# Optimization experiments

Measured on AMD Instinct MI355X. Metric: run time of the kernel, lower is better.

## Reference

```python
import jax, jax.numpy as jnp
import numpy as np

BETA = 0.2


def setup_inputs() -> dict:
    key = jax.random.key(0)
    k1, k2 = jax.random.split(key)
    B, C, H, W = 32, 64, 64, 64  # C == H == W required by the original reshape/permute
    K, D = 512, 64               # num_embeddings, embedding_dim (D == C)
    quant_input = jax.random.normal(k1, (B, C, H, W), dtype=jnp.float32)
    codebook = jax.random.normal(k2, (K, D), dtype=jnp.float32)
    return {"quant_input": quant_input, "codebook": codebook}


def reference(quant_input, codebook):
    B, C, H, W = quant_input.shape
    # (B,C,H,W) -> (B,HW,C)
    x = jnp.transpose(quant_input, (0, 2, 3, 1)).reshape(B, H * W, C)
    # squared euclidean distances (argmin identical to cdist argmin)
    x_sq = jnp.sum(x * x, axis=-1, keepdims=True)          # (B,HW,1)
    e_sq = jnp.sum(codebook * codebook, axis=-1)            # (K,)
    dist = x_sq - 2.0 * jnp.einsum('bnd,kd->bnk', x, codebook) + e_sq  # (B,HW,K)
    encoding_indices = jnp.argmin(dist, axis=-1)            # (B,HW)
    # gather codes, then the original (buggy-but-faithful) reshape/permute
    quant_out = codebook[encoding_indices.reshape(-1)]      # (B*HW, D)
    quant_out = quant_out.reshape(quant_input.shape)        # (B,C,H,W) layout
    quant_out = jnp.transpose(quant_out, (0, 3, 1, 2))      # (B,W,C,H)
    commitment_loss = jnp.mean((jax.lax.stop_gradient(quant_out) - quant_input) ** 2)
    codebook_loss = jnp.mean((quant_out - jax.lax.stop_gradient(quant_input)) ** 2)
    loss = codebook_loss + BETA * commitment_loss
    # straight-through estimator
    quant_out = quant_input + jax.lax.stop_gradient(quant_out - quant_input)
    encoding_indices = encoding_indices.reshape(-1, quant_out.shape[-2], quant_out.shape[-1])
    return quant_out, loss, encoding_indices
```

## Files before the change

### kernel.cpp

```cpp
#include <hip/hip_runtime.h>
#include <math.h>

#define K_CODES 512
#define DIM 64
#define NPTS (32 * 4096)
#define NQ (NPTS * DIM)
#define BPTS 128
#define TAU 2.0e-3f

typedef _Float16 f16x8 __attribute__((ext_vector_type(8)));
typedef float f32x4 __attribute__((ext_vector_type(4)));


__global__ void finalize_kernel(float* __restrict__ loss) {
    loss[0] = 1.2f * loss[0] / 8388608.0f;
}

__global__ __launch_bounds__(64) void prep_kernel(const float* __restrict__ cb,
                                                  _Float16* __restrict__ blob,
                                                  float* __restrict__ shalfg,
                                                  float* __restrict__ loss) {
    int k = blockIdx.x, d = threadIdx.x;
    if (k == 0 && d == 0) loss[0] = 0.0f;
    float e = cb[k * DIM + d];
    _Float16 hi = (_Float16)e;
    _Float16 lo = (_Float16)(e - (float)hi);
    int cf = k >> 4, col = k & 15;
    int q = d >> 5, dd = d & 31, kg = dd >> 3, j = dd & 7;
    size_t base = ((size_t)(cf * 4 + q) * 64 + (kg * 16 + col)) * 8 + j;
    blob[base] = hi;
    blob[base + 2 * 64 * 8] = lo;
    float s = e * e;
#pragma unroll
    for (int m = 32; m; m >>= 1) s += __shfl_xor(s, m);
    if (d == 0) shalfg[k] = 0.5f * s;
}

__global__ __launch_bounds__(256, 1) void vq_fused(const float* __restrict__ qin,
                                                   const float* __restrict__ cb,
                                                   const _Float16* __restrict__ blob,
                                                   const float* __restrict__ shalfg,
                                                   float* __restrict__ out,
                                                   float* __restrict__ loss_acc,
                                                   float* __restrict__ idx_out) {
    __shared__ float shs[K_CODES];
    __shared__ int sfinal[BPTS];
    __shared__ float wsum[4];

    const int tid = threadIdx.x, lane = tid & 63, w = tid >> 6;
    const int row16 = lane & 15, kg = lane >> 4;
    const int wp = w * 32;
    const int n0 = blockIdx.x * BPTS;
    const int b = n0 >> 12, hw0 = n0 & 4095;
    const float* qbase = qin + ((size_t)b << 18) + hw0;
    const f16x8* blp = (const f16x8*)blob + lane;

    shs[tid] = shalfg[tid];
    shs[tid + 256] = shalfg[tid + 256];

    f16x8 ah0[2], ah1[2], al0[2], al1[2];
#pragma unroll
    for (int rr = 0; rr < 2; ++rr) {
        const float* xb = qbase + (wp + rr * 16 + row16);
#pragma unroll
        for (int j = 0; j < 8; ++j) {
            float xa = xb[(size_t)(kg * 8 + j) << 12];
            float xc = xb[(size_t)(32 + kg * 8 + j) << 12];
            _Float16 ha = (_Float16)xa, hc = (_Float16)xc;
            ah0[rr][j] = ha; al0[rr][j] = (_Float16)(xa - (float)ha);
            ah1[rr][j] = hc; al1[rr][j] = (_Float16)(xc - (float)hc);
        }
    }
    __syncthreads();

    float b1[8], b2[8];
    int k1[8];
#pragma unroll
    for (int sl = 0; sl < 8; ++sl) { b1[sl] = -INFINITY; b2[sl] = -INFINITY; k1[sl] = 0; }

#define LOADB(P0, P1, P2, P3, CF)              \
    {                                          \
        P0 = blp[((CF) * 4 + 0) * 64];         \
        P1 = blp[((CF) * 4 + 1) * 64];         \
        P2 = blp[((CF) * 4 + 2) * 64];         \
        P3 = blp[((CF) * 4 + 3) * 64];         \
    }
#define CONSUME(CF, B0, B1, BL0, BL1)                                              \
    {                                                                              \
        float sh = shs[(CF) * 16 + row16];                                         \
        f32x4 acA0 = {-sh, -sh, -sh, -sh}, acB0 = {0.f, 0.f, 0.f, 0.f};            \
        f32x4 acA1 = acA0, acB1 = acB0;                                            \
        acA0 = __builtin_amdgcn_mfma_f32_16x16x32_f16(ah0[0], B0, acA0, 0, 0, 0);  \
        acB0 = __builtin_amdgcn_mfma_f32_16x16x32_f16(al0[0], B0, acB0, 0, 0, 0);  \
        acA1 = __builtin_amdgcn_mfma_f32_16x16x32_f16(ah0[1], B0, acA1, 0, 0, 0);  \
        acB1 = __builtin_amdgcn_mfma_f32_16x16x32_f16(al0[1], B0, acB1, 0, 0, 0);  \
        acA0 = __builtin_amdgcn_mfma_f32_16x16x32_f16(ah1[0], B1, acA0, 0, 0, 0);  \
        acB0 = __builtin_amdgcn_mfma_f32_16x16x32_f16(al1[0], B1, acB0, 0, 0, 0);  \
        acA1 = __builtin_amdgcn_mfma_f32_16x16x32_f16(ah1[1], B1, acA1, 0, 0, 0);  \
        acB1 = __builtin_amdgcn_mfma_f32_16x16x32_f16(al1[1], B1, acB1, 0, 0, 0);  \
        acA0 = __builtin_amdgcn_mfma_f32_16x16x32_f16(ah0[0], BL0, acA0, 0, 0, 0); \
        acB0 = __builtin_amdgcn_mfma_f32_16x16x32_f16(ah1[0], BL1, acB0, 0, 0, 0); \
        acA1 = __builtin_amdgcn_mfma_f32_16x16x32_f16(ah0[1], BL0, acA1, 0, 0, 0); \
        acB1 = __builtin_amdgcn_mfma_f32_16x16x32_f16(ah1[1], BL1, acB1, 0, 0, 0); \
        const int kglob = (CF) * 16 + row16;                                       \
        _Pragma("unroll") for (int r = 0; r < 4; ++r) {                            \
            float s_ = acA0[r] + acB0[r];                                          \
            float o1 = b1[r];                                                      \
            bool c1 = s_ > o1;                                                     \
            b2[r] = __builtin_amdgcn_fmed3f(s_, o1, b2[r]);                        \
            b1[r] = c1 ? s_ : o1;                                                  \
            k1[r] = c1 ? kglob : k1[r];                                            \
        }                                                                          \
        _Pragma("unroll") for (int r = 0; r < 4; ++r) {                            \
            float s_ = acA1[r] + acB1[r];                                          \
            float o1 = b1[4 + r];                                                  \
            bool c1 = s_ > o1;                                                     \
            b2[4 + r] = __builtin_amdgcn_fmed3f(s_, o1, b2[4 + r]);                \
            b1[4 + r] = c1 ? s_ : o1;                                              \
            k1[4 + r] = c1 ? kglob : k1[4 + r];                                    \
        }                                                                          \
    }

    f16x8 pa0, pa1, pa2, pa3, qa0, qa1, qa2, qa3;
    LOADB(pa0, pa1, pa2, pa3, 0)
#pragma unroll 1
    for (int cf = 0; cf < 32; cf += 2) {
        LOADB(qa0, qa1, qa2, qa3, cf + 1)
        CONSUME(cf, pa0, pa1, pa2, pa3)
        if (cf + 2 < 32) LOADB(pa0, pa1, pa2, pa3, cf + 2)
        CONSUME(cf + 1, qa0, qa1, qa2, qa3)
    }
#undef LOADB
#undef CONSUME

#pragma unroll
    for (int m = 1; m <= 8; m <<= 1) {
#pragma unroll
        for (int sl = 0; sl < 8; ++sl) {
            float ob1 = __shfl_xor(b1[sl], m);
            float ob2 = __shfl_xor(b2[sl], m);
            int ok1 = __shfl_xor(k1[sl], m);
            float nb2 = fmaxf(fminf(b1[sl], ob1), fmaxf(b2[sl], ob2));
            bool take = (ob1 > b1[sl]) || (ob1 == b1[sl] && ok1 < k1[sl]);
            b1[sl] = take ? ob1 : b1[sl];
            k1[sl] = take ? ok1 : k1[sl];
            b2[sl] = nb2;
        }
    }

#pragma unroll 1
    for (int sl = 0; sl < 8; ++sl) {
        bool fl = (row16 == 0) && ((b1[sl] - b2[sl]) < TAU);
        int pt = wp + (sl >> 2) * 16 + kg * 4 + (sl & 3);
        if (row16 == 0) sfinal[pt] = k1[sl];
        unsigned long long mask = __ballot(fl);
        while (mask) {
            int src = __ffsll((long long)mask) - 1;
            mask &= mask - 1;
            int rpt = wp + (sl >> 2) * 16 + ((src >> 4) << 2) + (sl & 3);
            const float* qx = qbase + rpt;
            float x[DIM];
#pragma unroll
            for (int d = 0; d < DIM; ++d) x[d] = qx[(size_t)d << 12];
            float bs = -INFINITY;
            int bi = 0;
#pragma unroll 1
            for (int i2 = 0; i2 < 8; ++i2) {
                int k = i2 * 64 + lane;
                const float4* c4 = (const float4*)(cb + (size_t)k * DIM);
                float d0 = 0.f, d1 = 0.f, d2 = 0.f, d3 = 0.f;
#pragma unroll
                for (int j = 0; j < 16; ++j) {
                    float4 c = c4[j];
                    d0 = fmaf(x[4 * j + 0], c.x, d0);
                    d1 = fmaf(x[4 * j + 1], c.y, d1);
                    d2 = fmaf(x[4 * j + 2], c.z, d2);
                    d3 = fmaf(x[4 * j + 3], c.w, d3);
                }
                float sc = ((d0 + d1) + (d2 + d3)) - shs[k];
                if (sc > bs) { bs = sc; bi = k; }
            }
#pragma unroll
            for (int m = 1; m < 64; m <<= 1) {
                float os = __shfl_xor(bs, m);
                int oi = __shfl_xor(bi, m);
                if (os > bs || (os == bs && oi < bi)) { bs = os; bi = oi; }
            }
            if (lane == 0) sfinal[rpt] = bi;
        }
    }
    __syncthreads();

    if (tid < BPTS) idx_out[n0 + tid] = (float)sfinal[tid];

    {
        int p = tid & 127, hh = tid >> 7;
        int ci = sfinal[p];
        const float* crow = cb + (size_t)ci * DIM + hh * 32;
        const float* qrow = qbase + p + ((size_t)(hh * 32) << 12);
        float* orow = out + ((size_t)b << 18) + hw0 + p + ((size_t)(hh * 32) << 12);
        float l0 = 0.f, l1 = 0.f, l2 = 0.f, l3 = 0.f;
#pragma unroll
        for (int d = 0; d < 32; d += 4) {
            float4 v = *(const float4*)(crow + d);
            orow[(size_t)(d + 0) << 12] = v.x;
            orow[(size_t)(d + 1) << 12] = v.y;
            orow[(size_t)(d + 2) << 12] = v.z;
            orow[(size_t)(d + 3) << 12] = v.w;
            float q0 = qrow[(size_t)(d + 0) << 12];
            float q1 = qrow[(size_t)(d + 1) << 12];
            float q2 = qrow[(size_t)(d + 2) << 12];
            float q3 = qrow[(size_t)(d + 3) << 12];
            float e0 = v.x - q0, e1 = v.y - q1, e2 = v.z - q2, e3 = v.w - q3;
            l0 = fmaf(e0, e0, l0); l1 = fmaf(e1, e1, l1);
            l2 = fmaf(e2, e2, l2); l3 = fmaf(e3, e3, l3);
        }
        float s = (l0 + l1) + (l2 + l3);
#pragma unroll
        for (int off = 32; off > 0; off >>= 1) s += __shfl_down(s, off);
        if (lane == 0) wsum[w] = s;
    }
    __syncthreads();
    if (tid == 0) atomicAdd(loss_acc, (wsum[0] + wsum[1]) + (wsum[2] + wsum[3]));
}

extern "C" void kernel_launch(void* const* d_in, const int* in_sizes, int n_in,
                              void* d_out, int out_size, void* d_ws, size_t ws_size,
                              hipStream_t stream) {
    const float* qin = (const float*)d_in[0];
    const float* cb = (const float*)d_in[1];
    float* out = (float*)d_out;
    float* loss_out = out + NQ;
    float* idx_out = out + NQ + 1;

    _Float16* blob = (_Float16*)d_ws;
    float* shalfg = (float*)((char*)d_ws + 131072);

    prep_kernel<<<K_CODES, 64, 0, stream>>>(cb, blob, shalfg, loss_out);
    vq_fused<<<NPTS / BPTS, 256, 0, stream>>>(qin, cb, blob, shalfg, out, loss_out, idx_out);
    finalize_kernel<<<1, 1, 0, stream>>>(loss_out);
}
```

Before: 70.20 us.

## Defer fp32 tie-break recheck of ambiguous points to a separate fixup kernel

Ambiguous points, whose fp16 top-two scores fall within a small margin, were previously re-scored in fp32 inside the main fused kernel, which stalled whole blocks. The main kernel now writes provisional indices and tags ambiguous ones with a negative encoding. A new fixup kernel scans all points, recomputes the argmin in fp32 for the tagged ones, and patches the index, the output row and the loss by a delta. This removes divergent serial work from the main kernel, at the cost of an extra launch that reads the whole index array and does scattered corrective writes.

```diff
diff --git a/kernel.cpp b/kernel.cpp
--- a/kernel.cpp
+++ b/kernel.cpp
@@ -148,50 +148,16 @@
         }
     }
 
-#pragma unroll 1
-    for (int sl = 0; sl < 8; ++sl) {
-        bool fl = (row16 == 0) && ((b1[sl] - b2[sl]) < TAU);
-        int pt = wp + (sl >> 2) * 16 + kg * 4 + (sl & 3);
-        if (row16 == 0) sfinal[pt] = k1[sl];
-        unsigned long long mask = __ballot(fl);
-        while (mask) {
-            int src = __ffsll((long long)mask) - 1;
-            mask &= mask - 1;
-            int rpt = wp + (sl >> 2) * 16 + ((src >> 4) << 2) + (sl & 3);
-            const float* qx = qbase + rpt;
-            float x[DIM];
-#pragma unroll
-            for (int d = 0; d < DIM; ++d) x[d] = qx[(size_t)d << 12];
-            float bs = -INFINITY;
-            int bi = 0;
-#pragma unroll 1
-            for (int i2 = 0; i2 < 8; ++i2) {
-                int k = i2 * 64 + lane;
-                const float4* c4 = (const float4*)(cb + (size_t)k * DIM);
-                float d0 = 0.f, d1 = 0.f, d2 = 0.f, d3 = 0.f;
-#pragma unroll
-                for (int j = 0; j < 16; ++j) {
-                    float4 c = c4[j];
-                    d0 = fmaf(x[4 * j + 0], c.x, d0);
-                    d1 = fmaf(x[4 * j + 1], c.y, d1);
-                    d2 = fmaf(x[4 * j + 2], c.z, d2);
-                    d3 = fmaf(x[4 * j + 3], c.w, d3);
-                }
-                float sc = ((d0 + d1) + (d2 + d3)) - shs[k];
-                if (sc > bs) { bs = sc; bi = k; }
-            }
-#pragma unroll
-            for (int m = 1; m < 64; m <<= 1) {
-                float os = __shfl_xor(bs, m);
-                int oi = __shfl_xor(bi, m);
-                if (os > bs || (os == bs && oi < bi)) { bs = os; bi = oi; }
-            }
-            if (lane == 0) sfinal[rpt] = bi;
+    if (row16 == 0) {
+#pragma unroll
+        for (int sl = 0; sl < 8; ++sl) {
+            int pt = wp + (sl >> 2) * 16 + kg * 4 + (sl & 3);
+            sfinal[pt] = k1[sl];
+            bool fl = (b1[sl] - b2[sl]) < TAU;
+            idx_out[n0 + pt] = fl ? -(float)(k1[sl] + 1) : (float)k1[sl];
         }
     }
     __syncthreads();
-
-    if (tid < BPTS) idx_out[n0 + tid] = (float)sfinal[tid];
 
     {
         int p = tid & 127, hh = tid >> 7;
@@ -224,6 +190,65 @@
     if (tid == 0) atomicAdd(loss_acc, (wsum[0] + wsum[1]) + (wsum[2] + wsum[3]));
 }
 
+__global__ __launch_bounds__(64, 1) void vq_fixup(const float* __restrict__ qin,
+                                                  const float* __restrict__ cb,
+                                                  const float* __restrict__ shalfg,
+                                                  float* __restrict__ idx_out,
+                                                  float* __restrict__ out,
+                                                  float* __restrict__ loss_acc) {
+    const int lane = threadIdx.x;
+    const int nb = blockIdx.x * 64;
+    float v = idx_out[nb + lane];
+    unsigned long long mask = __ballot(v < 0.0f);
+    while (mask) {
+        int src = __ffsll((long long)mask) - 1;
+        mask &= mask - 1;
+        int n = nb + src;
+        int oldk = (int)(-__shfl(v, src)) - 1;
+        int b = n >> 12, hw = n & 4095;
+        const float* qx = qin + ((size_t)b << 18) + hw;
+        float x[DIM];
+#pragma unroll
+        for (int d = 0; d < DIM; ++d) x[d] = qx[(size_t)d << 12];
+        float bs = -INFINITY;
+        int bi = 0;
+#pragma unroll 1
+        for (int i2 = 0; i2 < 8; ++i2) {
+            int k = i2 * 64 + lane;
+            const float4* c4 = (const float4*)(cb + (size_t)k * DIM);
+            float d0 = 0.f, d1 = 0.f, d2 = 0.f, d3 = 0.f;
+#pragma unroll
+            for (int j = 0; j < 16; ++j) {
+                float4 c = c4[j];
+                d0 = fmaf(x[4 * j + 0], c.x, d0);
+                d1 = fmaf(x[4 * j + 1], c.y, d1);
+                d2 = fmaf(x[4 * j + 2], c.z, d2);
+                d3 = fmaf(x[4 * j + 3], c.w, d3);
+            }
+            float sc = ((d0 + d1) + (d2 + d3)) - shalfg[k];
+            if (sc > bs) { bs = sc; bi = k; }
+        }
+#pragma unroll
+        for (int m = 1; m < 64; m <<= 1) {
+            float os = __shfl_xor(bs, m);
+            int oi = __shfl_xor(bi, m);
+            if (os > bs || (os == bs && oi < bi)) { bs = os; bi = oi; }
+        }
+        if (lane == 0) idx_out[n] = (float)bi;
+        if (bi != oldk) {
+            float xd = x[lane];
+            float nv = cb[(size_t)bi * DIM + lane];
+            float ov = cb[(size_t)oldk * DIM + lane];
+            float en = nv - xd, eo = ov - xd;
+            float delta = en * en - eo * eo;
+#pragma unroll
+            for (int m = 32; m > 0; m >>= 1) delta += __shfl_down(delta, m);
+            out[((size_t)b << 18) + ((size_t)lane << 12) + hw] = nv;
+            if (lane == 0) atomicAdd(loss_acc, delta);
+        }
+    }
+}
+
 extern "C" void kernel_launch(void* const* d_in, const int* in_sizes, int n_in,
                               void* d_out, int out_size, void* d_ws, size_t ws_size,
                               hipStream_t stream) {
@@ -238,5 +263,6 @@
 
     prep_kernel<<<K_CODES, 64, 0, stream>>>(cb, blob, shalfg, loss_out);
     vq_fused<<<NPTS / BPTS, 256, 0, stream>>>(qin, cb, blob, shalfg, out, loss_out, idx_out);
+    vq_fixup<<<NPTS / 64, 64, 0, stream>>>(qin, cb, shalfg, idx_out, out, loss_out);
     finalize_kernel<<<1, 1, 0, stream>>>(loss_out);
 }
```

Result: slower. 72.65 us (+3.5%).
